# Performance work log

Hardware: AMD Instinct MI355X
Metric: run time of the kernel (lower is better)

## Reference

```python
import jax, jax.numpy as jnp
import numpy as np

DAMPING = 0.9998  # from __init__ default


def setup_inputs() -> dict:
    key = jax.random.key(0)
    ks = jax.random.split(key, 6)
    B, M, D, T = 2, 64, 64, 8192
    forces = jax.random.normal(ks[0], (B, M, D, T), jnp.float32) * 0.01
    home_modifier = jax.random.normal(ks[1], (B, M, D, T), jnp.float32) * 0.1
    mic = jax.random.normal(ks[2], (B, M, D, 1), jnp.float32)
    # learned parameters, sized/initialized as in the torch module
    masses = jax.random.uniform(ks[3], (M,), jnp.float32, minval=1000.0, maxval=10000.0)
    tensions = jax.random.uniform(ks[4], (M, D), jnp.float32, minval=20.0, maxval=30.0)
    gains = jax.random.uniform(ks[5], (M,), jnp.float32, minval=10.0, maxval=100.0)
    return {"forces": forces, "home_modifier": home_modifier, "mic": mic,
            "masses": masses, "tensions": tensions, "gains": gains}


def reference(forces, home_modifier, mic, masses, tensions, gains):
    # forces, home_modifier: [B, M, D, T]; mic: [B, M, D, 1]
    B, M, D, T = forces.shape
    mic3 = mic[..., 0]                 # [B, M, D] readout vector per mass
    tens = tensions[None]              # [1, M, D]
    inv_mass = 1.0 / masses[None, :, None]   # [1, M, 1]
    gain = gains[None, :, None]        # [1, M, 1]
    # home buffer is zeros, so h = home + home_modifier = home_modifier
    f_t = jnp.moveaxis(forces, -1, 0)          # [T, B, M, D]
    h_t = jnp.moveaxis(home_modifier, -1, 0)   # [T, B, M, D]

    def step(carry, inp):
        pos, vel = carry
        f, h = inp
        acc = f + tens * (h - pos) * inv_mass
        vel = (vel + acc) * DAMPING
        pos = pos + vel
        # tanh readout contracted against mic over dimension axis -> [B, M]
        r = jnp.sum(jnp.tanh(vel * gain) * mic3, axis=-1)
        return (pos, vel), r

    zero = jnp.zeros((B, M, D), forces.dtype)
    (_, _), rec = jax.lax.scan(step, (zero, zero), (f_t, h_t))  # rec: [T, B, M]
    return jnp.moveaxis(rec, 0, 2)[..., None]  # [B, M, T, 1]
```

## Files before the change

kernel.cpp:

```cpp
#include <hip/hip_runtime.h>
#include <hip/hip_fp16.h>

#define DAMPF 0.9998f

constexpr int T_len = 8192;
constexpr int NCH   = 64;
constexpr int CHLEN = T_len / NCH;
constexpr int TT    = 32;
constexpr int NTILE = CHLEN / TT;
constexpr int SF    = TT + 1;

constexpr size_t VEL_BYTES = (size_t)128 * T_len * 64 * 2;
constexpr size_t WS_NEEDED = VEL_BYTES + (size_t)128 * NCH * 128 * 4;

template<bool WV>
__global__ __launch_bounds__(128) void goo_pass1(
    const float* __restrict__ F, const float* __restrict__ H,
    const float* __restrict__ tens, const float* __restrict__ mass,
    float* __restrict__ states, uint32_t* __restrict__ vb)
{
  __shared__ float ftile[2][64*SF];
  __shared__ float htile[2][64*SF];
  const int widx = threadIdx.x >> 6;
  const int lane = threadIdx.x & 63;
  const int w    = blockIdx.x * 2 + widx;
  const int bm   = w >> 6;
  const int c    = w & (NCH - 1);
  const int m    = bm & 63;
  const float k  = tens[m*64 + lane] / mass[m];

  float* ftw = ftile[widx];
  float* htw = htile[widx];
  const int r8 = lane >> 3;
  const int c4 = (lane & 7) * 4;
  const int la = r8*SF + c4;
  const size_t gbase = (size_t)bm * 64 * T_len + (size_t)c * CHLEN
                     + (size_t)r8 * T_len + c4;
  const float* Fp = F + gbase;
  const float* Hp = H + gbase;
  const int dbase = lane * SF;
  uint32_t* vstore = WV ? (vb + (((size_t)bm*(T_len/2) + (size_t)c*(CHLEN/2))*64 + lane))
                        : nullptr;

  float4 pf[8], ph[8];
  auto load_tile = [&](int toff) {
    #pragma unroll
    for (int i = 0; i < 8; ++i) {
      pf[i] = *(const float4*)(Fp + (size_t)(8*i) * T_len + toff);
      ph[i] = *(const float4*)(Hp + (size_t)(8*i) * T_len + toff);
    }
  };
  auto store_tile = [&]() {
    #pragma unroll
    for (int i = 0; i < 8; ++i) {
      const int a = la + 8*i*SF;
      ftw[a+0]=pf[i].x; ftw[a+1]=pf[i].y; ftw[a+2]=pf[i].z; ftw[a+3]=pf[i].w;
      htw[a+0]=ph[i].x; htw[a+1]=ph[i].y; htw[a+2]=ph[i].z; htw[a+3]=ph[i].w;
    }
  };

  float pos = 0.f, vel = 0.f, prev = 0.f;
  load_tile(0);
  for (int tt = 0; tt < NTILE; ++tt) {
    store_tile();
    __builtin_amdgcn_wave_barrier();
    if (tt + 1 < NTILE) load_tile((tt+1)*TT);
    #pragma unroll
    for (int t = 0; t < TT; ++t) {
      float ff = ftw[dbase + t];
      float hh = htw[dbase + t];
      float acc = fmaf(k, hh - pos, ff);
      vel = (vel + acc) * DAMPF;
      pos += vel;
      if (WV) {
        if (t & 1) {
          __half2 h2 = __floats2half2_rn(prev, vel);
          vstore[(size_t)((tt*TT + t) >> 1) * 64] = __builtin_bit_cast(uint32_t, h2);
        } else {
          prev = vel;
        }
      }
    }
    __builtin_amdgcn_wave_barrier();
  }
  const size_t slot = ((size_t)bm*NCH + c) * 128;
  states[slot + lane]      = pos;
  states[slot + 64 + lane] = vel;
}

__global__ __launch_bounds__(256) void goo_combine(
    const float* __restrict__ tens, const float* __restrict__ mass,
    float* __restrict__ states)
{
  const int tid = blockIdx.x * 256 + threadIdx.x;
  const int bm  = tid >> 6;
  const int d   = tid & 63;
  const int m   = bm & 63;
  const double k  = (double)tens[m*64 + d] / (double)mass[m];
  const double Dd = 0.9998;
  double a00 = 1.0 - Dd*k, a01 = Dd, a10 = -Dd*k, a11 = Dd;
  #pragma unroll
  for (int i = 0; i < 7; ++i) {
    double b00 = a00*a00 + a01*a10;
    double b01 = a00*a01 + a01*a11;
    double b10 = a10*a00 + a11*a10;
    double b11 = a10*a01 + a11*a11;
    a00=b00; a01=b01; a10=b10; a11=b11;
  }
  double xp = 0.0, xv = 0.0;
  for (int c = 0; c < NCH; ++c) {
    const size_t base = ((size_t)bm*NCH + c)*128 + d;
    const float zp = states[base];
    const float zv = states[base + 64];
    states[base]      = (float)xp;
    states[base + 64] = (float)xv;
    const double np = a00*xp + a01*xv + (double)zp;
    const double nv = a10*xp + a11*xv + (double)zv;
    xp = np; xv = nv;
  }
}

__global__ __launch_bounds__(256) void goo_pass2_fast(
    const uint32_t* __restrict__ vb, const float* __restrict__ states,
    const float* __restrict__ mic, const float* __restrict__ mass,
    const float* __restrict__ tens, const float* __restrict__ gains,
    float* __restrict__ out)
{
  const int lane = threadIdx.x & 63;
  const int w    = blockIdx.x * 4 + (threadIdx.x >> 6);
  const int bm   = w >> 6;
  const int c    = w & (NCH - 1);
  const int m    = bm & 63;
  const float k       = tens[m*64 + lane] / mass[m];
  const float Dk      = DAMPF * k;
  const float pregain = 2.0f * gains[m];
  const float micv    = mic[bm*64 + lane];
  const float m2n     = -2.0f * micv;

  const size_t slot = ((size_t)bm*NCH + c) * 128;
  float wp = states[slot + lane];
  float wv = states[slot + 64 + lane];
  const uint32_t* vp = vb + (((size_t)bm*(T_len/2) + (size_t)c*(CHLEN/2))*64 + lane);
  const bool odd = lane & 1;

  for (int half = 0; half < 2; ++half) {
    float keep = 0.f;
    #pragma unroll 8
    for (int j = 0; j < 32; ++j) {
      const uint32_t pk = vp[(size_t)(half*32 + j) * 64];
      const __half2 h2 = __builtin_bit_cast(__half2, pk);
      const float2 vpair = __half22float2(h2);
      wv = fmaf(-Dk, wp, DAMPF*wv); wp += wv;
      const float va = vpair.x + wv;
      wv = fmaf(-Dk, wp, DAMPF*wv); wp += wv;
      const float vbv = vpair.y + wv;
      const float ya = fmaf(m2n, __builtin_amdgcn_rcpf(__expf(va *pregain) + 1.f), micv);
      const float yb = fmaf(m2n, __builtin_amdgcn_rcpf(__expf(vbv*pregain) + 1.f), micv);
      const float d0 = odd ? yb : ya;
      const float e0 = __shfl_xor(odd ? ya : yb, 1);
      float f = d0 + e0;
      f += __shfl_xor(f, 2);
      f += __shfl_xor(f, 4);
      f += __shfl_xor(f, 8);
      f += __shfl_xor(f, 16);
      f += __shfl_xor(f, 32);
      keep = (lane == 2*j + (int)odd) ? f : keep;
    }
    out[(size_t)bm*T_len + c*CHLEN + half*64 + lane] = keep;
  }
}

__global__ __launch_bounds__(128) void goo_pass2_slow(
    const float* __restrict__ F, const float* __restrict__ H,
    const float* __restrict__ mic, const float* __restrict__ mass,
    const float* __restrict__ tens, const float* __restrict__ gains,
    const float* __restrict__ states, float* __restrict__ out)
{
  __shared__ float ftile[2][64*SF];
  __shared__ float htile[2][64*SF];
  const int widx = threadIdx.x >> 6;
  const int lane = threadIdx.x & 63;
  const int w    = blockIdx.x * 2 + widx;
  const int bm   = w >> 6;
  const int c    = w & (NCH - 1);
  const int m    = bm & 63;
  const float k       = tens[m*64 + lane] / mass[m];
  const float pregain = 2.0f * gains[m];
  const float micv    = mic[bm*64 + lane];
  const float m2n     = -2.0f * micv;

  float* ftw = ftile[widx];
  float* htw = htile[widx];
  const int r8 = lane >> 3;
  const int c4 = (lane & 7) * 4;
  const int la = r8*SF + c4;
  const size_t gbase = (size_t)bm * 64 * T_len + (size_t)c * CHLEN
                     + (size_t)r8 * T_len + c4;
  const float* Fp = F + gbase;
  const float* Hp = H + gbase;
  const int dbase = lane * SF;

  float4 pf[8], ph[8];
  auto load_tile = [&](int toff) {
    #pragma unroll
    for (int i = 0; i < 8; ++i) {
      pf[i] = *(const float4*)(Fp + (size_t)(8*i) * T_len + toff);
      ph[i] = *(const float4*)(Hp + (size_t)(8*i) * T_len + toff);
    }
  };
  auto store_tile = [&]() {
    #pragma unroll
    for (int i = 0; i < 8; ++i) {
      const int a = la + 8*i*SF;
      ftw[a+0]=pf[i].x; ftw[a+1]=pf[i].y; ftw[a+2]=pf[i].z; ftw[a+3]=pf[i].w;
      htw[a+0]=ph[i].x; htw[a+1]=ph[i].y; htw[a+2]=ph[i].z; htw[a+3]=ph[i].w;
    }
  };

  const size_t slot = ((size_t)bm*NCH + c) * 128;
  float pos = states[slot + lane];
  float vel = states[slot + 64 + lane];

  float keep = 0.f;
  load_tile(0);
  for (int tt = 0; tt < NTILE; ++tt) {
    store_tile();
    __builtin_amdgcn_wave_barrier();
    if (tt + 1 < NTILE) load_tile((tt+1)*TT);
    #pragma unroll
    for (int t = 0; t < TT; ++t) {
      float ff = ftw[dbase + t];
      float hh = htw[dbase + t];
      float acc = fmaf(k, hh - pos, ff);
      vel = (vel + acc) * DAMPF;
      pos += vel;
      float e  = __expf(vel * pregain);
      float rr = __builtin_amdgcn_rcpf(e + 1.0f);
      float y  = fmaf(m2n, rr, micv);
      y += __shfl_xor(y, 1);
      y += __shfl_xor(y, 2);
      y += __shfl_xor(y, 4);
      y += __shfl_xor(y, 8);
      y += __shfl_xor(y, 16);
      y += __shfl_xor(y, 32);
      const int tmod = (tt & 1) * TT + t;
      keep = (lane == tmod) ? y : keep;
    }
    __builtin_amdgcn_wave_barrier();
    if (tt & 1) {
      out[(size_t)bm*T_len + c*CHLEN + (tt>>1)*64 + lane] = keep;
    }
  }
}

extern "C" void kernel_launch(void* const* d_in, const int* in_sizes, int n_in,
                              void* d_out, int out_size, void* d_ws, size_t ws_size,
                              hipStream_t stream)
{
  const float* F    = (const float*)d_in[0];
  const float* H    = (const float*)d_in[1];
  const float* mic  = (const float*)d_in[2];
  const float* mass = (const float*)d_in[3];
  const float* tens = (const float*)d_in[4];
  const float* gain = (const float*)d_in[5];
  float* out = (float*)d_out;

  const bool fast = ws_size >= WS_NEEDED;
  if (fast) {
    uint32_t* vb   = (uint32_t*)d_ws;
    float* states  = (float*)((char*)d_ws + VEL_BYTES);
    goo_pass1<true><<<4096, 128, 0, stream>>>(F, H, tens, mass, states, vb);
    goo_combine   <<<  32, 256, 0, stream>>>(tens, mass, states);
    goo_pass2_fast<<<2048, 256, 0, stream>>>(vb, states, mic, mass, tens, gain, out);
  } else {
    float* states = (float*)d_ws;
    goo_pass1<false><<<4096, 128, 0, stream>>>(F, H, tens, mass, states, nullptr);
    goo_combine   <<<  32, 256, 0, stream>>>(tens, mass, states);
    goo_pass2_slow<<<4096, 128, 0, stream>>>(F, H, mic, mass, tens, gain, states, out);
  }
}
```

Measured before the change: 181.2 us.

## Precombine force and home input into one LDS tile and batch velocity stores

Folds the force and home-modifier inputs into a single pre-scaled term when the tile is staged to LDS. This halves LDS traffic and shortens the serial recurrence to two FMAs plus an add. Velocity half2 stores are buffered in registers and written after each tile, and launch bounds now request occupancy 4. The reassociation changes floating-point rounding slightly, and the extra pk registers add register pressure.

```diff
diff --git a/kernel.cpp b/kernel.cpp
--- a/kernel.cpp
+++ b/kernel.cpp
@@ -14,23 +14,22 @@
 constexpr size_t WS_NEEDED = VEL_BYTES + (size_t)128 * NCH * 128 * 4;
 
 template<bool WV>
-__global__ __launch_bounds__(128) void goo_pass1(
+__global__ __launch_bounds__(128, 4) void goo_pass1(
     const float* __restrict__ F, const float* __restrict__ H,
     const float* __restrict__ tens, const float* __restrict__ mass,
     float* __restrict__ states, uint32_t* __restrict__ vb)
 {
-  __shared__ float ftile[2][64*SF];
-  __shared__ float htile[2][64*SF];
+  __shared__ float utile[2][64*SF];
   const int widx = threadIdx.x >> 6;
   const int lane = threadIdx.x & 63;
   const int w    = blockIdx.x * 2 + widx;
   const int bm   = w >> 6;
   const int c    = w & (NCH - 1);
   const int m    = bm & 63;
-  const float k  = tens[m*64 + lane] / mass[m];
-
-  float* ftw = ftile[widx];
-  float* htw = htile[widx];
+  const float invm = 1.0f / mass[m];
+  const float kD   = DAMPF * tens[m*64 + lane] * invm;
+
+  float* utw = utile[widx];
   const int r8 = lane >> 3;
   const int c4 = (lane & 7) * 4;
   const int la = r8*SF + c4;
@@ -42,6 +41,10 @@
   uint32_t* vstore = WV ? (vb + (((size_t)bm*(T_len/2) + (size_t)c*(CHLEN/2))*64 + lane))
                         : nullptr;
 
+  float kD8[8];
+  #pragma unroll
+  for (int i = 0; i < 8; ++i) kD8[i] = DAMPF * tens[m*64 + r8 + 8*i] * invm;
+
   float4 pf[8], ph[8];
   auto load_tile = [&](int toff) {
     #pragma unroll
@@ -54,8 +57,10 @@
     #pragma unroll
     for (int i = 0; i < 8; ++i) {
       const int a = la + 8*i*SF;
-      ftw[a+0]=pf[i].x; ftw[a+1]=pf[i].y; ftw[a+2]=pf[i].z; ftw[a+3]=pf[i].w;
-      htw[a+0]=ph[i].x; htw[a+1]=ph[i].y; htw[a+2]=ph[i].z; htw[a+3]=ph[i].w;
+      utw[a+0] = fmaf(kD8[i], ph[i].x, DAMPF*pf[i].x);
+      utw[a+1] = fmaf(kD8[i], ph[i].y, DAMPF*pf[i].y);
+      utw[a+2] = fmaf(kD8[i], ph[i].z, DAMPF*pf[i].z);
+      utw[a+3] = fmaf(kD8[i], ph[i].w, DAMPF*pf[i].w);
     }
   };
 
@@ -65,21 +70,26 @@
     store_tile();
     __builtin_amdgcn_wave_barrier();
     if (tt + 1 < NTILE) load_tile((tt+1)*TT);
+    uint32_t pk[16];
     #pragma unroll
     for (int t = 0; t < TT; ++t) {
-      float ff = ftw[dbase + t];
-      float hh = htw[dbase + t];
-      float acc = fmaf(k, hh - pos, ff);
-      vel = (vel + acc) * DAMPF;
+      const float uD = utw[dbase + t];
+      const float wrk = fmaf(-kD, pos, uD);
+      vel = fmaf(DAMPF, vel, wrk);
       pos += vel;
       if (WV) {
         if (t & 1) {
           __half2 h2 = __floats2half2_rn(prev, vel);
-          vstore[(size_t)((tt*TT + t) >> 1) * 64] = __builtin_bit_cast(uint32_t, h2);
+          pk[t >> 1] = __builtin_bit_cast(uint32_t, h2);
         } else {
           prev = vel;
         }
       }
+    }
+    if (WV) {
+      #pragma unroll
+      for (int jj = 0; jj < 16; ++jj)
+        vstore[(size_t)(tt*16 + jj) * 64] = pk[jj];
     }
     __builtin_amdgcn_wave_barrier();
   }
```

After: 186.9 us. 3.1% more time.

## Load pass1 tiles directly into LDS with XOR-swizzled layout and explicit vmcnt pipelining

Applied to the files above, without the earlier changes.

Pass 1 now runs one wave per block and fetches each 64-step tile of forces and home_modifier straight from global memory into shared memory using global_load_lds. An XOR swizzle replaces the padded layout so each lane can read float4 rows without bank conflicts. Velocity halves are buffered in registers and written out per tile, and explicit waitcnt and sched barriers overlap the second tile's loads with the first tile's stores. The per-step arithmetic is also refactored so the damping factor is folded into k. This removes the register round trip and scalar LDS stores, but leaves only two tiles per chunk, uses 32KB of LDS per wave, and relies on hand-written vmcnt counts being correct.

```diff
diff --git a/kernel.cpp b/kernel.cpp
--- a/kernel.cpp
+++ b/kernel.cpp
@@ -6,83 +6,101 @@
 constexpr int T_len = 8192;
 constexpr int NCH   = 64;
 constexpr int CHLEN = T_len / NCH;
-constexpr int TT    = 32;
-constexpr int NTILE = CHLEN / TT;
-constexpr int SF    = TT + 1;
+constexpr int PTT   = 64;
 
 constexpr size_t VEL_BYTES = (size_t)128 * T_len * 64 * 2;
 constexpr size_t WS_NEEDED = VEL_BYTES + (size_t)128 * NCH * 128 * 4;
 
+#define GLD_LDS16(g, l) __builtin_amdgcn_global_load_lds( \
+    (const __attribute__((address_space(1))) void*)(g),   \
+    (__attribute__((address_space(3))) void*)(l), 16, 0, 0)
+
 template<bool WV>
-__global__ __launch_bounds__(128) void goo_pass1(
+__global__ __launch_bounds__(64) void goo_pass1(
     const float* __restrict__ F, const float* __restrict__ H,
     const float* __restrict__ tens, const float* __restrict__ mass,
     float* __restrict__ states, uint32_t* __restrict__ vb)
 {
-  __shared__ float ftile[2][64*SF];
-  __shared__ float htile[2][64*SF];
-  const int widx = threadIdx.x >> 6;
-  const int lane = threadIdx.x & 63;
-  const int w    = blockIdx.x * 2 + widx;
+  __shared__ float fbuf[64*64];
+  __shared__ float hbuf[64*64];
+  const int lane = threadIdx.x;
+  const int w    = blockIdx.x;
   const int bm   = w >> 6;
   const int c    = w & (NCH - 1);
   const int m    = bm & 63;
-  const float k  = tens[m*64 + lane] / mass[m];
-
-  float* ftw = ftile[widx];
-  float* htw = htile[widx];
-  const int r8 = lane >> 3;
-  const int c4 = (lane & 7) * 4;
-  const int la = r8*SF + c4;
-  const size_t gbase = (size_t)bm * 64 * T_len + (size_t)c * CHLEN
-                     + (size_t)r8 * T_len + c4;
-  const float* Fp = F + gbase;
-  const float* Hp = H + gbase;
-  const int dbase = lane * SF;
+  const float kD = DAMPF * tens[m*64 + lane] / mass[m];
+
+  const int rl = lane >> 4;
+  const int gl = lane & 15;
+  const size_t chunkbase = (size_t)bm*64*T_len + (size_t)c*CHLEN;
   uint32_t* vstore = WV ? (vb + (((size_t)bm*(T_len/2) + (size_t)c*(CHLEN/2))*64 + lane))
                         : nullptr;
 
-  float4 pf[8], ph[8];
-  auto load_tile = [&](int toff) {
-    #pragma unroll
-    for (int i = 0; i < 8; ++i) {
-      pf[i] = *(const float4*)(Fp + (size_t)(8*i) * T_len + toff);
-      ph[i] = *(const float4*)(Hp + (size_t)(8*i) * T_len + toff);
-    }
-  };
-  auto store_tile = [&]() {
-    #pragma unroll
-    for (int i = 0; i < 8; ++i) {
-      const int a = la + 8*i*SF;
-      ftw[a+0]=pf[i].x; ftw[a+1]=pf[i].y; ftw[a+2]=pf[i].z; ftw[a+3]=pf[i].w;
-      htw[a+0]=ph[i].x; htw[a+1]=ph[i].y; htw[a+2]=ph[i].z; htw[a+3]=ph[i].w;
+  auto issue_tile = [&](int tile) {
+    const int t0 = tile * PTT;
+    #pragma unroll
+    for (int i = 0; i < 16; ++i) {
+      const int r    = 4*i + rl;
+      const int gsrc = gl ^ (r & 15);
+      const size_t goff = chunkbase + (size_t)r*T_len + t0 + 4*gsrc;
+      GLD_LDS16(F + goff, &fbuf[i*256]);
+      GLD_LDS16(H + goff, &hbuf[i*256]);
     }
   };
 
   float pos = 0.f, vel = 0.f, prev = 0.f;
-  load_tile(0);
-  for (int tt = 0; tt < NTILE; ++tt) {
-    store_tile();
-    __builtin_amdgcn_wave_barrier();
-    if (tt + 1 < NTILE) load_tile((tt+1)*TT);
-    #pragma unroll
-    for (int t = 0; t < TT; ++t) {
-      float ff = ftw[dbase + t];
-      float hh = htw[dbase + t];
-      float acc = fmaf(k, hh - pos, ff);
-      vel = (vel + acc) * DAMPF;
-      pos += vel;
-      if (WV) {
-        if (t & 1) {
-          __half2 h2 = __floats2half2_rn(prev, vel);
-          vstore[(size_t)((tt*TT + t) >> 1) * 64] = __builtin_bit_cast(uint32_t, h2);
-        } else {
-          prev = vel;
+  uint32_t pk[32];
+
+  auto compute_tile = [&](int tile) {
+    #pragma unroll
+    for (int j = 0; j < 16; ++j) {
+      const int gaddr = 64*lane + 4*(j ^ (lane & 15));
+      const float4 f4 = *(const float4*)&fbuf[gaddr];
+      const float4 h4 = *(const float4*)&hbuf[gaddr];
+      const float fs[4] = {f4.x, f4.y, f4.z, f4.w};
+      const float hs[4] = {h4.x, h4.y, h4.z, h4.w};
+      #pragma unroll
+      for (int q = 0; q < 4; ++q) {
+        const int tl = 4*j + q;
+        const float uD = fmaf(kD, hs[q], DAMPF*fs[q]);
+        vel = fmaf(DAMPF, vel, fmaf(-kD, pos, uD));
+        pos += vel;
+        if (WV) {
+          if (tl & 1) {
+            __half2 h2 = __floats2half2_rn(prev, vel);
+            pk[tl >> 1] = __builtin_bit_cast(uint32_t, h2);
+          } else {
+            prev = vel;
+          }
         }
       }
     }
-    __builtin_amdgcn_wave_barrier();
-  }
+  };
+  auto store_tile = [&](int tile) {
+    #pragma unroll
+    for (int jj = 0; jj < 32; ++jj)
+      vstore[(size_t)(tile*32 + jj) * 64] = pk[jj];
+  };
+
+  issue_tile(0);
+  asm volatile("s_waitcnt vmcnt(0)" ::: "memory");
+  __builtin_amdgcn_sched_barrier(0);
+  compute_tile(0);
+  __builtin_amdgcn_sched_barrier(0);
+  issue_tile(1);
+  __builtin_amdgcn_sched_barrier(0);
+  if (WV) store_tile(0);
+  __builtin_amdgcn_sched_barrier(0);
+  if constexpr (WV) {
+    asm volatile("s_waitcnt vmcnt(32)" ::: "memory");
+  } else {
+    asm volatile("s_waitcnt vmcnt(0)" ::: "memory");
+  }
+  __builtin_amdgcn_sched_barrier(0);
+  compute_tile(1);
+  __builtin_amdgcn_sched_barrier(0);
+  if (WV) store_tile(1);
+
   const size_t slot = ((size_t)bm*NCH + c) * 128;
   states[slot + lane]      = pos;
   states[slot + 64 + lane] = vel;
@@ -170,6 +188,10 @@
   }
 }
 
+constexpr int TT = 32;
+constexpr int NTILE = CHLEN / TT;
+constexpr int SF = TT + 1;
+
 __global__ __launch_bounds__(128) void goo_pass2_slow(
     const float* __restrict__ F, const float* __restrict__ H,
     const float* __restrict__ mic, const float* __restrict__ mass,
@@ -269,12 +291,12 @@
   if (fast) {
     uint32_t* vb   = (uint32_t*)d_ws;
     float* states  = (float*)((char*)d_ws + VEL_BYTES);
-    goo_pass1<true><<<4096, 128, 0, stream>>>(F, H, tens, mass, states, vb);
+    goo_pass1<true><<<8192, 64, 0, stream>>>(F, H, tens, mass, states, vb);
     goo_combine   <<<  32, 256, 0, stream>>>(tens, mass, states);
     goo_pass2_fast<<<2048, 256, 0, stream>>>(vb, states, mic, mass, tens, gain, out);
   } else {
     float* states = (float*)d_ws;
-    goo_pass1<false><<<4096, 128, 0, stream>>>(F, H, tens, mass, states, nullptr);
+    goo_pass1<false><<<8192, 64, 0, stream>>>(F, H, tens, mass, states, nullptr);
     goo_combine   <<<  32, 256, 0, stream>>>(tens, mass, states);
     goo_pass2_slow<<<4096, 128, 0, stream>>>(F, H, mic, mass, tens, gain, states, out);
   }
```

After: 178.3 us. Within noise of the previous version (-1.6%).
